# Kernel tuning notes

Hardware: AMD Instinct MI355X
Metric: run time of the kernel (lower is better)

The kernel has to match this reference:

```python
import jax, jax.numpy as jnp
import numpy as np
from jax import lax

# Architecture constants (match init_kwargs)
B = 4          # clips
T_SEG = 8      # num_segments
D_IN = 256
D_HID = 64
H = 112
W = 112
WIN_T = 5      # window[0], temporal
WIN_S = 9      # window[1] == window[2], spatial
MAXD = WIN_S // 2


def setup_inputs() -> dict:
    key = jax.random.key(0)
    k1, k2, k3, k4 = jax.random.split(key, 4)
    x = jax.random.normal(k1, (B * T_SEG, D_IN, H, W), jnp.float32)
    conv_w = jax.random.normal(k2, (D_HID, D_IN, 3, 3), jnp.float32) * 0.05
    bn_gamma = jnp.ones((D_HID,), jnp.float32)
    bn_beta = jnp.zeros((D_HID,), jnp.float32)
    bn_mean = jax.random.normal(k3, (D_HID,), jnp.float32) * 0.1
    bn_var = jax.random.uniform(k4, (D_HID,), jnp.float32, minval=0.5, maxval=1.5)
    return {"x": x, "conv_w": conv_w, "bn_gamma": bn_gamma, "bn_beta": bn_beta,
            "bn_mean": bn_mean, "bn_var": bn_var}


def reference(x, conv_w, bn_gamma, bn_beta, bn_mean, bn_var):
    # downsample: Conv2d(k=3, s=2, p=1, no bias) + BatchNorm2d (eval) + ReLU
    y = lax.conv_general_dilated(x, conv_w, window_strides=(2, 2),
                                 padding=((1, 1), (1, 1)),
                                 dimension_numbers=("NCHW", "OIHW", "NCHW"))
    scale = bn_gamma / jnp.sqrt(bn_var + 1e-5)
    y = jax.nn.relu((y - bn_mean[:, None, None]) * scale[:, None, None]
                    + bn_beta[:, None, None])
    bt, c, h, w = y.shape
    b = bt // T_SEG
    y = y.reshape(b, T_SEG, c, h, w)
    # per-frame, per-pixel L2 normalization over channels (eps=1e-6, as in _L2normalize)
    yn = y / jnp.sqrt(jnp.sum(y * y, axis=2, keepdims=True) + 1e-6)
    # temporal zero-pad (padded frames normalize to 0 in the original too: 0/sqrt(eps)=0)
    half_t = WIN_T // 2
    ypad = jnp.pad(yn, ((0, 0), (half_t, half_t), (0, 0), (0, 0), (0, 0)))
    # spatial zero-pad by max displacement
    ypad = jnp.pad(ypad, ((0, 0), (0, 0), (0, 0), (MAXD, MAXD), (MAXD, MAXD)))
    # temporal windows: f2[b, t, l] = padded frame t+l   -> (b, T, L, c, h+2m, w+2m)
    f2 = jnp.stack([ypad[:, l:l + T_SEG] for l in range(WIN_T)], axis=2)
    # local windowed correlation (equivalent to einsum + _corr_abs_to_rel):
    # out[b,t,l,u,v,h,w] = sum_c yn[b,t,c,h,w] * f2[b,t,l,c,h+u,w+v]
    corrs = []
    for u in range(WIN_S):
        for v in range(WIN_S):
            corrs.append(jnp.einsum("btchw,btlchw->btlhw",
                                     yn, f2[:, :, :, :, u:u + h, v:v + w]))
    corr = jnp.stack(corrs, axis=-1).reshape(b, T_SEG, WIN_T, h, w, WIN_S, WIN_S)
    # '(b t l) u v h w -> b t h w 1 l u v'
    corr = jnp.transpose(corr, (0, 1, 3, 4, 2, 5, 6))
    return corr[:, :, :, :, None, :, :, :]
```

## Files before the change

### kernel.cpp

```cpp
#include <hip/hip_runtime.h>
#include <hip/hip_bf16.h>

#define TSEG 8
#define NBC 4
#define NBT 32
#define CIN 256
#define CH 64
#define HIN 112
#define WIN_ 112
#define HO 56
#define WO 56
#define HPD 64
#define WPD 64

#define FRSZE ((size_t)(HPD * WPD * CH))
#define ZF_U   147456
#define FR_U   (ZF_U + 262144)
#define WS_TOTAL_BYTES ((size_t)(FR_U + 32 * 262144) * 2)

typedef __attribute__((ext_vector_type(8))) short bf16x8;
typedef __attribute__((ext_vector_type(4))) float f32x4;

__device__ __forceinline__ unsigned short f2bf(float f) {
    union { float f; unsigned u; } c; c.f = f;
    unsigned u = c.u + 0x7fffu + ((c.u >> 16) & 1u);
    return (unsigned short)(u >> 16);
}

__global__ __launch_bounds__(256) void wprep_k(
    const float* __restrict__ w, unsigned short* __restrict__ wpp)
{
    int e = blockIdx.x * 256 + threadIdx.x;
    int cout = e / 2304;
    int rem  = e - cout * 2304;
    int ci   = rem / 9;
    int tap  = rem - ci * 9;
    wpp[((size_t)tap * 64 + cout) * 256 + ci] = f2bf(w[e]);
}

__global__ __launch_bounds__(256) void conv_mfma_k(
    const float* __restrict__ x, const unsigned short* __restrict__ wpp,
    const float* __restrict__ gamma, const float* __restrict__ beta,
    const float* __restrict__ mean, const float* __restrict__ var,
    unsigned short* __restrict__ frames)
{
    __shared__ unsigned short in_lds[5 * 120 * 32];
    __shared__ float sq[2][2][64];

    const int tid  = threadIdx.x;
    const int lane = tid & 63;
    const int wv   = tid >> 6;
    const int r    = wv >> 1;
    const int nh   = wv & 1;
    const int l15  = lane & 15;
    const int l4   = lane >> 4;
    const int hb   = blockIdx.x;
    const int bt   = blockIdx.y;

    const float* xb = x + (size_t)bt * (CIN * HIN * WIN_);

    f32x4 acc[4][2];
#pragma unroll
    for (int mt = 0; mt < 4; ++mt) {
        acc[mt][0] = (f32x4){0.f, 0.f, 0.f, 0.f};
        acc[mt][1] = (f32x4){0.f, 0.f, 0.f, 0.f};
    }

    int a_off[4][3];
#pragma unroll
    for (int mt = 0; mt < 4; ++mt) {
        int c = mt * 16 + l15; if (c > 55) c = 55;
#pragma unroll
        for (int kw = 0; kw < 3; ++kw) {
            int col = 2 * c + kw;
            int ba  = col * 64 + l4 * 16;
            ba ^= ((col >> 1) & 7) << 4;
            a_off[mt][kw] = ba;
        }
    }

    const unsigned short* bptr0 = wpp + ((size_t)(nh * 32 + l15) * 256 + l4 * 8);
    const unsigned short* bptr1 = wpp + ((size_t)(nh * 32 + 16 + l15) * 256 + l4 * 8);

    const int ih0 = 4 * hb - 1;

    for (int cb = 0; cb < 8; ++cb) {
        __syncthreads();
#pragma unroll
        for (int j = 0; j < 5; ++j) {
            const int jj  = wv + j * 4;
            const int row = jj >> 2, cig = jj & 3;
            const int ih  = ih0 + row;
            const int ihc = ih < 0 ? 0 : (ih > 111 ? 111 : ih);
            const float* xr = xb + ((size_t)(cb * 32 + cig * 8) * HIN + ihc) * WIN_;
            const bool rowin = (ih >= 0) && (ih < HIN);
#pragma unroll
            for (int p = 0; p < 2; ++p) {
                const int col = lane + p * 64;
                if (col < 113) {
                    const int iw  = col - 1;
                    const int iwc = iw < 0 ? 0 : iw;
                    const bool inb = rowin && (iw >= 0);
                    unsigned pk[4];
#pragma unroll
                    for (int q = 0; q < 4; ++q) {
                        float v0 = xr[(size_t)(2 * q) * HIN * WIN_ + iwc];
                        float v1 = xr[(size_t)(2 * q + 1) * HIN * WIN_ + iwc];
                        v0 = inb ? v0 : 0.f;
                        v1 = inb ? v1 : 0.f;
                        union { float f; unsigned u; } c0, c1; c0.f = v0; c1.f = v1;
                        unsigned u0 = c0.u + 0x7fffu + ((c0.u >> 16) & 1u);
                        unsigned u1 = c1.u + 0x7fffu + ((c1.u >> 16) & 1u);
                        pk[q] = (u0 >> 16) | (u1 & 0xffff0000u);
                    }
                    int ba = (row * 120 + col) * 64 + cig * 16;
                    ba ^= ((col >> 1) & 7) << 4;
                    *(uint4*)((char*)in_lds + ba) = make_uint4(pk[0], pk[1], pk[2], pk[3]);
                }
            }
        }
        __syncthreads();

        const int rowb = (2 * r) * 7680;
#pragma unroll
        for (int kh = 0; kh < 3; ++kh) {
            const int rb = rowb + kh * 7680;
#pragma unroll
            for (int kw = 0; kw < 3; ++kw) {
                const int tap = kh * 3 + kw;
                const bf16x8 bf0 = *(const bf16x8*)(bptr0 + tap * 16384 + cb * 32);
                const bf16x8 bf1 = *(const bf16x8*)(bptr1 + tap * 16384 + cb * 32);
#pragma unroll
                for (int mt = 0; mt < 4; ++mt) {
                    const bf16x8 af = *(const bf16x8*)((const char*)in_lds + (rb + a_off[mt][kw]));
                    acc[mt][0] = __builtin_amdgcn_mfma_f32_16x16x32_bf16(af, bf0, acc[mt][0], 0, 0, 0);
                    acc[mt][1] = __builtin_amdgcn_mfma_f32_16x16x32_bf16(af, bf1, acc[mt][1], 0, 0, 0);
                }
            }
        }
    }

    const int cout0 = nh * 32 + l15;
    const int cout1 = cout0 + 16;
    const float sc0 = gamma[cout0] * rsqrtf(var[cout0] + 1e-5f);
    const float bb0 = beta[cout0] - mean[cout0] * sc0;
    const float sc1 = gamma[cout1] * rsqrtf(var[cout1] + 1e-5f);
    const float bb1 = beta[cout1] - mean[cout1] * sc1;

    float yv[4][2][4];
    float ssr[4][4];
#pragma unroll
    for (int mt = 0; mt < 4; ++mt) {
#pragma unroll
        for (int reg = 0; reg < 4; ++reg) {
            float y0 = fmaxf(fmaf(acc[mt][0][reg], sc0, bb0), 0.f);
            float y1 = fmaxf(fmaf(acc[mt][1][reg], sc1, bb1), 0.f);
            yv[mt][0][reg] = y0; yv[mt][1][reg] = y1;
            float ss = y0 * y0 + y1 * y1;
            ss += __shfl_xor(ss, 1);
            ss += __shfl_xor(ss, 2);
            ss += __shfl_xor(ss, 4);
            ss += __shfl_xor(ss, 8);
            ssr[mt][reg] = ss;
        }
    }
    if (l15 == 0) {
#pragma unroll
        for (int mt = 0; mt < 4; ++mt)
#pragma unroll
            for (int reg = 0; reg < 4; ++reg)
                sq[r][nh][mt * 16 + l4 * 4 + reg] = ssr[mt][reg];
    }
    __syncthreads();

    const int h = 2 * hb + r;
    unsigned short* fdst = frames + (size_t)bt * FRSZE + (size_t)(h + 4) * WPD * CH;
#pragma unroll
    for (int mt = 0; mt < 4; ++mt) {
#pragma unroll
        for (int reg = 0; reg < 4; ++reg) {
            const int c = mt * 16 + l4 * 4 + reg;
            if (c < 56) {
                const float tot = sq[r][0][c] + sq[r][1][c];
                const float inv = rsqrtf(tot + 1e-6f);
                unsigned short* dp = fdst + (size_t)(c + 4) * CH;
                dp[cout0] = f2bf(yv[mt][0][reg] * inv);
                dp[cout1] = f2bf(yv[mt][1][reg] * inv);
            }
        }
    }
}

__global__ __launch_bounds__(64) void pad_k(float* __restrict__ out)
{
    const int lane = threadIdx.x;
    const int h = blockIdx.x;
    const int p = blockIdx.y;
    const int b = blockIdx.z;
    const int PT[6] = {0, 0, 1, 6, 7, 7};
    const int PL[6] = {0, 1, 0, 4, 3, 4};
    const int t = PT[p], l = PL[p];
    float* ob = out + (size_t)((b * TSEG + t) * HO + h) * (WO * 405) + l * 81;
#pragma unroll 4
    for (int w = 0; w < 56; ++w) {
        float* orow = ob + (size_t)w * 405;
        orow[lane] = 0.f;
        if (lane < 17) orow[lane + 64] = 0.f;
    }
}

__global__ __launch_bounds__(256) void corr_f_k(
    const unsigned short* __restrict__ frames, float* __restrict__ out)
{
    __shared__ unsigned short zl[9 * 4096];
    __shared__ float so[4][504];

    const int tid  = threadIdx.x;
    const int lane = tid & 63;
    const int wv   = tid >> 6;
    const int l15  = lane & 15;
    const int l4   = lane >> 4;
    const int w7   = lane / 9;
    const int v9   = lane - w7 * 9;

    const int h = blockIdx.x;
    const int f = blockIdx.y;
    const int b = blockIdx.z;

    const unsigned short* zb = frames + (size_t)(b * TSEG + f) * FRSZE
                             + (size_t)h * (WPD * CH);
#pragma unroll
    for (int k = 0; k < 18; ++k) {
        const int e   = tid + k * 256;
        const int row = e >> 9;
        const int c   = e & 511;
        const uint4 val = *(const uint4*)(zb + (size_t)row * 4096 + c * 8);
        const int ba = row * 8192 + ((c * 16) ^ (((c >> 3) & 7) << 4));
        *(uint4*)((char*)zl + ba) = val;
    }
    __syncthreads();

    int roff[4][2];
#pragma unroll
    for (int n = 0; n < 4; ++n) {
        const int px = n * 16 + l15;
#pragma unroll
        for (int hf = 0; hf < 2; ++hf)
            roff[n][hf] = (px * 128 + hf * 64 + l4 * 16) ^ ((px & 7) << 4);
    }

    const int PM[7] = {0, 0, 1, 1, 2, 2, 3};
    const int PN[7] = {0, 1, 1, 2, 2, 3, 3};
    float* sw = so[wv];

    for (int pass = 0; pass < 2; ++pass) {
        if (pass == 1 && wv != 0) break;
        const int l = (pass == 0) ? wv : 4;
        const int t = f + 2 - l;
        if (t < 0 || t > 7) continue;
        const int bt = b * TSEG + t;

        const unsigned short* yb = frames + (size_t)bt * FRSZE
                                 + (size_t)(h + 4) * (WPD * CH);
        bf16x8 yf[4][2];
#pragma unroll
        for (int m = 0; m < 4; ++m) {
            int wc = (m << 4) + l15; if (wc > 55) wc = 55;
            const unsigned short* ap = yb + (size_t)(wc + 4) * CH + (l4 << 3);
            yf[m][0] = *(const bf16x8*)(ap);
            yf[m][1] = *(const bf16x8*)(ap + 32);
        }

        float* ob = out + (size_t)(bt * HO + h) * (WO * 405) + l * 81;

#pragma unroll
        for (int u = 0; u < 9; ++u) {
            const char* rb = (const char*)zl + u * 8192;
            bf16x8 zf[4][2];
#pragma unroll
            for (int n = 0; n < 4; ++n) {
                zf[n][0] = *(const bf16x8*)(rb + roff[n][0]);
                zf[n][1] = *(const bf16x8*)(rb + roff[n][1]);
            }

            f32x4 acc[7];
#pragma unroll
            for (int i = 0; i < 7; ++i) acc[i] = (f32x4){0.f, 0.f, 0.f, 0.f};
#pragma unroll
            for (int i = 0; i < 7; ++i) {
                acc[i] = __builtin_amdgcn_mfma_f32_16x16x32_bf16(zf[PN[i]][0], yf[PM[i]][0], acc[i], 0, 0, 0);
                acc[i] = __builtin_amdgcn_mfma_f32_16x16x32_bf16(zf[PN[i]][1], yf[PM[i]][1], acc[i], 0, 0, 0);
            }

#pragma unroll
            for (int i = 0; i < 7; ++i) {
                const int w = (PM[i] << 4) + l15;
#pragma unroll
                for (int reg = 0; reg < 4; ++reg) {
                    const int zc = (PN[i] << 4) + (l4 << 2) + reg;
                    const int v  = zc - w;
                    if (w < 56 && (unsigned)v <= 8u)
                        sw[w * 9 + v] = acc[i][reg];
                }
            }

            if (w7 < 7) {
                float* obu = ob + u * 9;
#pragma unroll
                for (int it = 0; it < 8; ++it) {
                    const int w = it * 7 + w7;
                    obu[(size_t)w * 405 + v9] = sw[w * 9 + v9];
                }
            }
        }
    }
}

extern "C" void kernel_launch(void* const* d_in, const int* in_sizes, int n_in,
                              void* d_out, int out_size, void* d_ws, size_t ws_size,
                              hipStream_t stream)
{
    const float* x     = (const float*)d_in[0];
    const float* wgt   = (const float*)d_in[1];
    const float* gamma = (const float*)d_in[2];
    const float* beta  = (const float*)d_in[3];
    const float* mean  = (const float*)d_in[4];
    const float* var   = (const float*)d_in[5];
    float* out = (float*)d_out;

    unsigned short* wpp    = (unsigned short*)d_ws;
    unsigned short* frames = wpp + FR_U;

    if (ws_size < WS_TOTAL_BYTES) return;

    hipMemsetAsync(d_ws, 0, WS_TOTAL_BYTES, stream);
    wprep_k<<<dim3(576), 256, 0, stream>>>(wgt, wpp);
    conv_mfma_k<<<dim3(28, NBT), 256, 0, stream>>>(x, wpp, gamma, beta, mean, var, frames);
    pad_k<<<dim3(56, 6, NBC), 64, 0, stream>>>(out);
    corr_f_k<<<dim3(56, TSEG, NBC), 256, 0, stream>>>(frames, out);
}
```

Measured before the change: 278.5 us.

## Use five-wave corr blocks with direct stores and vectorize conv input staging

The correlation kernel now launches 320 threads so each of the five temporal offsets gets its own wave, instead of wave 0 doing a serial second pass. It also drops the LDS staging buffer and writes MFMA results straight to global memory with scattered stores. The conv input loader reads float2 pairs per lane and zeros the left pad column once instead of clamping per element. The aim is to remove the serialized fifth pass and LDS round-trips, at the cost of less coalesced global writes from the correlation kernel.

```diff
diff --git a/kernel.cpp b/kernel.cpp
--- a/kernel.cpp
+++ b/kernel.cpp
@@ -22,9 +22,12 @@
 typedef __attribute__((ext_vector_type(4))) float f32x4;
 
 __device__ __forceinline__ unsigned short f2bf(float f) {
-    union { float f; unsigned u; } c; c.f = f;
-    unsigned u = c.u + 0x7fffu + ((c.u >> 16) & 1u);
-    return (unsigned short)(u >> 16);
+    __hip_bfloat16 h = __float2bfloat16(f);
+    union { __hip_bfloat16 h; unsigned short u; } c; c.h = h;
+    return c.u;
+}
+__device__ __forceinline__ unsigned pk2bf(float lo, float hi) {
+    return (unsigned)f2bf(lo) | ((unsigned)f2bf(hi) << 16);
 }
 
 __global__ __launch_bounds__(256) void wprep_k(
@@ -84,39 +87,41 @@
 
     const int ih0 = 4 * hb - 1;
 
+    if (tid < 20) {
+        const int row = tid >> 2, cig = tid & 3;
+        const int ba = (row * 120) * 64 + cig * 16;
+        *(uint4*)((char*)in_lds + ba) = make_uint4(0u, 0u, 0u, 0u);
+    }
+
     for (int cb = 0; cb < 8; ++cb) {
         __syncthreads();
-#pragma unroll
-        for (int j = 0; j < 5; ++j) {
-            const int jj  = wv + j * 4;
-            const int row = jj >> 2, cig = jj & 3;
-            const int ih  = ih0 + row;
-            const int ihc = ih < 0 ? 0 : (ih > 111 ? 111 : ih);
-            const float* xr = xb + ((size_t)(cb * 32 + cig * 8) * HIN + ihc) * WIN_;
-            const bool rowin = (ih >= 0) && (ih < HIN);
-#pragma unroll
-            for (int p = 0; p < 2; ++p) {
-                const int col = lane + p * 64;
-                if (col < 113) {
-                    const int iw  = col - 1;
-                    const int iwc = iw < 0 ? 0 : iw;
-                    const bool inb = rowin && (iw >= 0);
-                    unsigned pk[4];
+        if (lane < 56) {
+#pragma unroll
+            for (int j = 0; j < 5; ++j) {
+                const int jj  = wv + j * 4;
+                const int row = jj >> 2, cig = jj & 3;
+                const int ih  = ih0 + row;
+                unsigned pkA[4], pkB[4];
+                if (ih >= 0 && ih < HIN) {
+                    const float* xr = xb + ((size_t)(cb * 32 + cig * 8) * HIN + ih) * WIN_
+                                    + 2 * lane;
 #pragma unroll
                     for (int q = 0; q < 4; ++q) {
-                        float v0 = xr[(size_t)(2 * q) * HIN * WIN_ + iwc];
-                        float v1 = xr[(size_t)(2 * q + 1) * HIN * WIN_ + iwc];
-                        v0 = inb ? v0 : 0.f;
-                        v1 = inb ? v1 : 0.f;
-                        union { float f; unsigned u; } c0, c1; c0.f = v0; c1.f = v1;
-                        unsigned u0 = c0.u + 0x7fffu + ((c0.u >> 16) & 1u);
-                        unsigned u1 = c1.u + 0x7fffu + ((c1.u >> 16) & 1u);
-                        pk[q] = (u0 >> 16) | (u1 & 0xffff0000u);
+                        const float2 va = *(const float2*)(xr + (size_t)(2 * q) * (HIN * WIN_));
+                        const float2 vb = *(const float2*)(xr + (size_t)(2 * q + 1) * (HIN * WIN_));
+                        pkA[q] = pk2bf(va.x, vb.x);
+                        pkB[q] = pk2bf(va.y, vb.y);
                     }
-                    int ba = (row * 120 + col) * 64 + cig * 16;
-                    ba ^= ((col >> 1) & 7) << 4;
-                    *(uint4*)((char*)in_lds + ba) = make_uint4(pk[0], pk[1], pk[2], pk[3]);
+                } else {
+#pragma unroll
+                    for (int q = 0; q < 4; ++q) { pkA[q] = 0u; pkB[q] = 0u; }
                 }
+                const int colA = 1 + 2 * lane;
+                const int colB = colA + 1;
+                int baA = (row * 120 + colA) * 64 + cig * 16; baA ^= ((colA >> 1) & 7) << 4;
+                int baB = (row * 120 + colB) * 64 + cig * 16; baB ^= ((colB >> 1) & 7) << 4;
+                *(uint4*)((char*)in_lds + baA) = make_uint4(pkA[0], pkA[1], pkA[2], pkA[3]);
+                *(uint4*)((char*)in_lds + baB) = make_uint4(pkB[0], pkB[1], pkB[2], pkB[3]);
             }
         }
         __syncthreads();
@@ -209,19 +214,16 @@
     }
 }
 
-__global__ __launch_bounds__(256) void corr_f_k(
+__global__ __launch_bounds__(320) void corr_f5_k(
     const unsigned short* __restrict__ frames, float* __restrict__ out)
 {
     __shared__ unsigned short zl[9 * 4096];
-    __shared__ float so[4][504];
 
     const int tid  = threadIdx.x;
     const int lane = tid & 63;
     const int wv   = tid >> 6;
     const int l15  = lane & 15;
     const int l4   = lane >> 4;
-    const int w7   = lane / 9;
-    const int v9   = lane - w7 * 9;
 
     const int h = blockIdx.x;
     const int f = blockIdx.y;
@@ -230,15 +232,22 @@
     const unsigned short* zb = frames + (size_t)(b * TSEG + f) * FRSZE
                              + (size_t)h * (WPD * CH);
 #pragma unroll
-    for (int k = 0; k < 18; ++k) {
-        const int e   = tid + k * 256;
-        const int row = e >> 9;
-        const int c   = e & 511;
-        const uint4 val = *(const uint4*)(zb + (size_t)row * 4096 + c * 8);
-        const int ba = row * 8192 + ((c * 16) ^ (((c >> 3) & 7) << 4));
-        *(uint4*)((char*)zl + ba) = val;
+    for (int k = 0; k < 15; ++k) {
+        const int e = tid + k * 320;
+        if (e < 4608) {
+            const int row = e >> 9;
+            const int c   = e & 511;
+            const uint4 val = *(const uint4*)(zb + (size_t)row * 4096 + c * 8);
+            const int ba = row * 8192 + ((c * 16) ^ (((c >> 3) & 7) << 4));
+            *(uint4*)((char*)zl + ba) = val;
+        }
     }
     __syncthreads();
+
+    const int l = wv;
+    const int t = f + 2 - l;
+    if (t < 0 || t > 7) return;
+    const int bt = b * TSEG + t;
 
     int roff[4][2];
 #pragma unroll
@@ -249,67 +258,51 @@
             roff[n][hf] = (px * 128 + hf * 64 + l4 * 16) ^ ((px & 7) << 4);
     }
 
+    const unsigned short* yb = frames + (size_t)bt * FRSZE
+                             + (size_t)(h + 4) * (WPD * CH);
+    bf16x8 yf[4][2];
+#pragma unroll
+    for (int m = 0; m < 4; ++m) {
+        int wc = (m << 4) + l15; if (wc > 55) wc = 55;
+        const unsigned short* ap = yb + (size_t)(wc + 4) * CH + (l4 << 3);
+        yf[m][0] = *(const bf16x8*)(ap);
+        yf[m][1] = *(const bf16x8*)(ap + 32);
+    }
+
+    float* ob = out + (size_t)(bt * HO + h) * (WO * 405) + l * 81;
+
     const int PM[7] = {0, 0, 1, 1, 2, 2, 3};
     const int PN[7] = {0, 1, 1, 2, 2, 3, 3};
-    float* sw = so[wv];
-
-    for (int pass = 0; pass < 2; ++pass) {
-        if (pass == 1 && wv != 0) break;
-        const int l = (pass == 0) ? wv : 4;
-        const int t = f + 2 - l;
-        if (t < 0 || t > 7) continue;
-        const int bt = b * TSEG + t;
-
-        const unsigned short* yb = frames + (size_t)bt * FRSZE
-                                 + (size_t)(h + 4) * (WPD * CH);
-        bf16x8 yf[4][2];
-#pragma unroll
-        for (int m = 0; m < 4; ++m) {
-            int wc = (m << 4) + l15; if (wc > 55) wc = 55;
-            const unsigned short* ap = yb + (size_t)(wc + 4) * CH + (l4 << 3);
-            yf[m][0] = *(const bf16x8*)(ap);
-            yf[m][1] = *(const bf16x8*)(ap + 32);
-        }
-
-        float* ob = out + (size_t)(bt * HO + h) * (WO * 405) + l * 81;
-
-#pragma unroll
-        for (int u = 0; u < 9; ++u) {
-            const char* rb = (const char*)zl + u * 8192;
-            bf16x8 zf[4][2];
-#pragma unroll
-            for (int n = 0; n < 4; ++n) {
-                zf[n][0] = *(const bf16x8*)(rb + roff[n][0]);
-                zf[n][1] = *(const bf16x8*)(rb + roff[n][1]);
-            }
-
-            f32x4 acc[7];
-#pragma unroll
-            for (int i = 0; i < 7; ++i) acc[i] = (f32x4){0.f, 0.f, 0.f, 0.f};
-#pragma unroll
-            for (int i = 0; i < 7; ++i) {
-                acc[i] = __builtin_amdgcn_mfma_f32_16x16x32_bf16(zf[PN[i]][0], yf[PM[i]][0], acc[i], 0, 0, 0);
-                acc[i] = __builtin_amdgcn_mfma_f32_16x16x32_bf16(zf[PN[i]][1], yf[PM[i]][1], acc[i], 0, 0, 0);
-            }
-
-#pragma unroll
-            for (int i = 0; i < 7; ++i) {
-                const int w = (PM[i] << 4) + l15;
+
+#pragma unroll
+    for (int u = 0; u < 9; ++u) {
+        const char* rb = (const char*)zl + u * 8192;
+        bf16x8 zf[4][2];
+#pragma unroll
+        for (int n = 0; n < 4; ++n) {
+            zf[n][0] = *(const bf16x8*)(rb + roff[n][0]);
+            zf[n][1] = *(const bf16x8*)(rb + roff[n][1]);
+        }
+
+        f32x4 acc[7];
+#pragma unroll
+        for (int i = 0; i < 7; ++i) acc[i] = (f32x4){0.f, 0.f, 0.f, 0.f};
+#pragma unroll
+        for (int i = 0; i < 7; ++i) {
+            acc[i] = __builtin_amdgcn_mfma_f32_16x16x32_bf16(zf[PN[i]][0], yf[PM[i]][0], acc[i], 0, 0, 0);
+            acc[i] = __builtin_amdgcn_mfma_f32_16x16x32_bf16(zf[PN[i]][1], yf[PM[i]][1], acc[i], 0, 0, 0);
+        }
+
+#pragma unroll
+        for (int i = 0; i < 7; ++i) {
+            const int w = (PM[i] << 4) + l15;
+            if (w < 56) {
+                float* orow = ob + (size_t)w * 405 + u * 9;
+                const int v0 = (PN[i] << 4) + (l4 << 2) - w;
 #pragma unroll
                 for (int reg = 0; reg < 4; ++reg) {
-                    const int zc = (PN[i] << 4) + (l4 << 2) + reg;
-                    const int v  = zc - w;
-                    if (w < 56 && (unsigned)v <= 8u)
-                        sw[w * 9 + v] = acc[i][reg];
-                }
-            }
-
-            if (w7 < 7) {
-                float* obu = ob + u * 9;
-#pragma unroll
-                for (int it = 0; it < 8; ++it) {
-                    const int w = it * 7 + w7;
-                    obu[(size_t)w * 405 + v9] = sw[w * 9 + v9];
+                    const int v = v0 + reg;
+                    if ((unsigned)v <= 8u) orow[v] = acc[i][reg];
                 }
             }
         }
@@ -337,5 +330,5 @@
     wprep_k<<<dim3(576), 256, 0, stream>>>(wgt, wpp);
     conv_mfma_k<<<dim3(28, NBT), 256, 0, stream>>>(x, wpp, gamma, beta, mean, var, frames);
     pad_k<<<dim3(56, 6, NBC), 64, 0, stream>>>(out);
-    corr_f_k<<<dim3(56, TSEG, NBC), 256, 0, stream>>>(frames, out);
-}
+    corr_f5_k<<<dim3(56, TSEG, NBC), 320, 0, stream>>>(frames, out);
+}
```

Result: slower. 293.1 us (+5.2%).
